# Kernel tuning notes

Hardware: AMD Instinct MI355X
Metric: run time of the kernel (lower is better)

The kernel has to match this reference:

```python
import jax, jax.numpy as jnp
import numpy as np

IN_C, HID, L, NN, BS, OUT = 32, 128, 4, 64, 512, 3
N = NN * BS  # total graph vertices
EPS_LN = 1e-5
EPS_SM = 1e-16  # PyG softmax eps


def setup_inputs() -> dict:
    key = jax.random.key(0)
    ks = jax.random.split(key, 16)
    E = 524288
    x = jax.random.normal(ks[0], (N, IN_C), dtype=jnp.float32)
    edge_index = jax.random.randint(ks[1], (2, E), 0, N, dtype=jnp.int64)
    s = 0.1
    # first GAT layer (in -> hidden)
    W0 = jax.random.normal(ks[2], (IN_C, HID), dtype=jnp.float32) * s
    att_src0 = jax.random.normal(ks[3], (HID,), dtype=jnp.float32) * s
    att_dst0 = jax.random.normal(ks[4], (HID,), dtype=jnp.float32) * s
    bias0 = jnp.zeros((HID,), dtype=jnp.float32)
    # residual GAT layers (hidden -> hidden), stacked over L
    W_res = jax.random.normal(ks[5], (L, HID, HID), dtype=jnp.float32) * s
    att_src_res = jax.random.normal(ks[6], (L, HID), dtype=jnp.float32) * s
    att_dst_res = jax.random.normal(ks[7], (L, HID), dtype=jnp.float32) * s
    bias_res = jnp.zeros((L, HID), dtype=jnp.float32)
    gamma = jnp.ones((L, HID), dtype=jnp.float32)
    beta = jnp.zeros((L, HID), dtype=jnp.float32)
    # per-node predictor heads
    W1p = jax.random.normal(ks[8], (NN, HID, HID // 2), dtype=jnp.float32) * s
    W2p = jax.random.normal(ks[9], (NN, HID // 2, OUT), dtype=jnp.float32) * s
    return {"x": x, "edge_index": edge_index, "W0": W0, "att_src0": att_src0,
            "att_dst0": att_dst0, "bias0": bias0, "W_res": W_res,
            "att_src_res": att_src_res, "att_dst_res": att_dst_res,
            "bias_res": bias_res, "gamma": gamma, "beta": beta,
            "W1p": W1p, "W2p": W2p}


def _gat(x, src, dst, W, a_src, a_dst, b):
    # PyG GATConv, heads=1, negative_slope=0.2, self-loops already appended
    h = x @ W                                   # [N, H]
    a_s = (h * a_src).sum(-1)                   # [N]
    a_d = (h * a_dst).sum(-1)                   # [N]
    e = jax.nn.leaky_relu(a_s[src] + a_d[dst], 0.2)   # [E]
    m = jax.ops.segment_max(e, dst, num_segments=N)
    e = jnp.exp(e - m[dst])
    z = jax.ops.segment_sum(e, dst, num_segments=N)
    alpha = e / (z[dst] + EPS_SM)               # [E]
    out = jax.ops.segment_sum(h[src] * alpha[:, None], dst, num_segments=N)
    return out + b


def _layernorm(x, g, b):
    mu = x.mean(-1, keepdims=True)
    var = ((x - mu) ** 2).mean(-1, keepdims=True)
    return (x - mu) * jax.lax.rsqrt(var + EPS_LN) * g + b


def reference(x, edge_index, W0, att_src0, att_dst0, bias0, W_res,
              att_src_res, att_dst_res, bias_res, gamma, beta, W1p, W2p):
    loops = jnp.arange(N, dtype=edge_index.dtype)
    src = jnp.concatenate([edge_index[0], loops])
    dst = jnp.concatenate([edge_index[1], loops])
    # first GAT + relu
    h = jax.nn.relu(_gat(x, src, dst, W0, att_src0, att_dst0, bias0))
    # res+ blocks: h = h + conv(dropout(act(norm(h))))  (dropout=identity, eval)
    for i in range(L):
        t = jax.nn.relu(_layernorm(h, gamma[i], beta[i]))
        t = _gat(t, src, dst, W_res[i], att_src_res[i], att_dst_res[i], bias_res[i])
        h = h + t
    h = jax.nn.relu(_layernorm(h, gamma[0], beta[0]))
    # per-node predictor heads
    h = h.reshape(NN, BS, HID)
    t = jax.nn.relu(jnp.einsum('nbh,nhk->nbk', h, W1p))
    logits = jnp.einsum('nbk,nko->nbo', t, W2p)
    return jax.nn.softmax(logits, axis=-1)   # softmax over class dim (dim=1 per node slice)
```

## Files before the change

### kernel.cpp

```cpp
#include <hip/hip_runtime.h>
#include <hip/hip_fp8.h>
#include <math.h>

#define NND   32768
#define HIDD  128
#define NHEAD 64
#define BSS   512
#define OUTC  3

typedef _Float16 half_t;
typedef __attribute__((ext_vector_type(8))) _Float16 half8;
typedef __attribute__((ext_vector_type(4))) float f32x4;

__device__ __forceinline__ unsigned enc_fp8x4(float a, float b, float c, float d) {
    __hip_fp8x4_e4m3 q(make_float4(a, b, c, d));
    return (unsigned)q.__x;
}
__device__ __forceinline__ float4 dec_fp8x4(unsigned v) {
    __hip_fp8x4_e4m3 t; t.__x = (__hip_fp8x4_storage_t)v;
    return (float4)t;
}

__global__ __launch_bounds__(256) void prep_kernel(const float* __restrict__ W0,
        const float* __restrict__ W_res, const float* __restrict__ W1p,
        const float* __restrict__ as0, const float* __restrict__ ad0,
        const float* __restrict__ as_res, const float* __restrict__ ad_res,
        const float* __restrict__ x, const int* __restrict__ ei, int E,
        half_t* __restrict__ Wh, half_t* __restrict__ W1h, half_t* __restrict__ W0t,
        float* __restrict__ wvec, half_t* __restrict__ xh,
        int* __restrict__ counts, int* __restrict__ rank) {
    int b = blockIdx.x, tid = threadIdx.x;
    if (b < 64) {
        __shared__ float tile[32][33];
        int l = b >> 4, t = b & 15;
        int k0 = (t >> 2) * 32, n0 = (t & 3) * 32;
        const float* src = W_res + (size_t)l * 128 * 128;
        half_t* dst = Wh + (size_t)l * 128 * 128;
        int c = tid & 31, r0 = tid >> 5;
#pragma unroll
        for (int i = 0; i < 4; ++i) tile[r0 + i * 8][c] = src[(size_t)(k0 + r0 + i * 8) * 128 + n0 + c];
        __syncthreads();
#pragma unroll
        for (int i = 0; i < 4; ++i) dst[(size_t)(n0 + r0 + i * 8) * 128 + k0 + c] = (half_t)tile[c][r0 + i * 8];
    } else if (b < 576) {
        __shared__ float tile[32][33];
        int bb = b - 64, head = bb >> 3, t = bb & 7;
        int k0 = (t >> 1) * 32, n0 = (t & 1) * 32;
        const float* src = W1p + (size_t)head * 128 * 64;
        half_t* dst = W1h + (size_t)head * 64 * 128;
        int c = tid & 31, r0 = tid >> 5;
#pragma unroll
        for (int i = 0; i < 4; ++i) tile[r0 + i * 8][c] = src[(size_t)(k0 + r0 + i * 8) * 64 + n0 + c];
        __syncthreads();
#pragma unroll
        for (int i = 0; i < 4; ++i) dst[(size_t)(n0 + r0 + i * 8) * 128 + k0 + c] = (half_t)tile[c][r0 + i * 8];
    } else if (b == 576) {
        __shared__ float t0[32][129];
        for (int i = tid; i < 4096; i += 256) t0[i >> 7][i & 127] = W0[i];
        __syncthreads();
        for (int i = tid; i < 4096; i += 256) { int n = i >> 5, k = i & 31; W0t[n * 32 + k] = (half_t)t0[k][n]; }
    } else if (b == 577) {
        for (int task = tid; task < 1088; task += 256) {
            const float* row; const float* att; int slot, sd;
            if (task < 64) {
                int k = task >> 1; sd = task & 1;
                row = W0 + k * 128; att = sd ? ad0 : as0; slot = k;
            } else {
                int tt = task - 64; int l = 1 + tt / 256; int r = tt % 256;
                int k = r >> 1; sd = r & 1;
                row = W_res + (size_t)(l - 1) * 16384 + k * 128;
                att = (sd ? ad_res : as_res) + (l - 1) * 128;
                slot = l * 128 + k;
            }
            float s = 0.f;
            for (int n = 0; n < 128; ++n) s += row[n] * att[n];
            (sd ? wvec + 640 : wvec)[slot] = s;
        }
    } else if (b < 1090) {
        int b2 = b - 578;
        const float* xs = x + (size_t)b2 * 64 * 32;
        half_t* xd = xh + (size_t)b2 * 64 * 32;
        for (int i = tid; i < 1024; i += 256) {
            float2 v = ((const float2*)xs)[i];
            union { unsigned u; half_t h[2]; } cv;
            cv.h[0] = (half_t)v.x; cv.h[1] = (half_t)v.y;
            ((unsigned*)xd)[i] = cv.u;
        }
    } else {
        int j = (b - 1090) * 256 + tid;
        int Etot = E + NND;
        if (j >= Etot) return;
        int dst = (j < E) ? ei[E + j] : (j - E);
        rank[j] = atomicAdd(&counts[dst], 1);
    }
}

__global__ __launch_bounds__(1024) void scan_kernel(const int* __restrict__ counts,
                                                    int* __restrict__ off) {
    __shared__ int sums[1024];
    int tid = threadIdx.x;
    int base = tid * 32;
    int tmp[32];
    int run = 0;
#pragma unroll
    for (int i = 0; i < 8; ++i) {
        int4 c4 = *(const int4*)&counts[base + i * 4];
        tmp[i*4+0] = run; run += c4.x;
        tmp[i*4+1] = run; run += c4.y;
        tmp[i*4+2] = run; run += c4.z;
        tmp[i*4+3] = run; run += c4.w;
    }
    sums[tid] = run;
    __syncthreads();
    for (int d = 1; d < 1024; d <<= 1) {
        int v = (tid >= d) ? sums[tid - d] : 0;
        __syncthreads();
        sums[tid] += v;
        __syncthreads();
    }
    int ebase = (tid == 0) ? 0 : sums[tid - 1];
#pragma unroll
    for (int i = 0; i < 32; ++i) off[base + i] = ebase + tmp[i];
    if (tid == 1023) off[NND] = sums[1023];
}

__global__ __launch_bounds__(256) void fill_a0_kernel(const int* __restrict__ ei, int E, int egrid,
        const int* __restrict__ off, const int* __restrict__ rank, int* __restrict__ csr_src,
        const half_t* __restrict__ xh, const float* __restrict__ wvec,
        float* __restrict__ a_s, float* __restrict__ a_d) {
    int b = blockIdx.x, tid = threadIdx.x;
    if (b < egrid) {
        int j = b * 256 + tid;
        int Etot = E + NND;
        if (j >= Etot) return;
        int src, dst;
        if (j < E) { src = ei[j]; dst = ei[E + j]; }
        else       { src = j - E; dst = j - E; }
        csr_src[off[dst] + rank[j]] = src;
    } else {
        __shared__ float ws0[32], wd0[32];
        if (tid < 32) { ws0[tid] = wvec[tid]; wd0[tid] = wvec[640 + tid]; }
        __syncthreads();
        int g = (b - egrid) * 256 + tid;
        int node = g >> 2, part = g & 3;
        half8 xv = *(const half8*)&xh[(size_t)node * 32 + part * 8];
        float s = 0.f, d2 = 0.f;
#pragma unroll
        for (int j = 0; j < 8; ++j) { float f = (float)xv[j]; s += f * ws0[part * 8 + j]; d2 += f * wd0[part * 8 + j]; }
        s += __shfl_xor(s, 1); s += __shfl_xor(s, 2);
        d2 += __shfl_xor(d2, 1); d2 += __shfl_xor(d2, 2);
        if (part == 0) { a_s[node] = s; a_d[node] = d2; }
    }
}

template <int K, bool RES>
__global__ __launch_bounds__(256) void fused_kernel(const void* __restrict__ srcdat,
        const float* __restrict__ a_sv, const float* __restrict__ a_dv,
        const int* __restrict__ csr_src, const int* __restrict__ off,
        const half_t* __restrict__ Whl, const float* __restrict__ bias,
        half_t* __restrict__ Hh, unsigned char* __restrict__ Th8o,
        const float* __restrict__ gamma, const float* __restrict__ beta,
        const float* __restrict__ wsn, const float* __restrict__ wdn,
        float* __restrict__ as_out, float* __restrict__ ad_out) {
    constexpr int KP = (K == 32) ? 40 : 136;
    __shared__ __align__(16) half_t Pt[16][KP];
    __shared__ __align__(16) float vv[16][132];
    int tid = threadIdx.x;
    int wv = tid >> 6, lane = tid & 63;
    int q = lane >> 4, r15 = lane & 15;
    int n0 = blockIdx.x * 16;

    for (int ln = wv * 4; ln < wv * 4 + 4; ++ln) {
        int d = n0 + ln;
        int beg = off[d], end = off[d + 1];
        float adv = a_dv[d];
        float pz = 0.f;
        if constexpr (K == 32) {
            const half_t* xh = (const half_t*)srcdat;
            float a0 = 0.f, a1 = 0.f;
            for (int base = beg; base < end; base += 64) {
                int j = base + lane;
                int s = 0; float p = 0.f;
                if (j < end) {
                    s = csr_src[j];
                    float t = a_sv[s] + adv;
                    t = (t > 0.f) ? t : 0.2f * t;
                    p = __expf(t);
                }
                pz += p;
                int cnt = end - base; if (cnt > 64) cnt = 64;
                int full = cnt & ~15;
                int k4 = 0;
                for (; k4 < full; k4 += 16) {
                    int s0 = __shfl(s, k4 + q);      float p0 = __shfl(p, k4 + q);
                    int s1 = __shfl(s, k4 + 4 + q);  float p1 = __shfl(p, k4 + 4 + q);
                    int s2 = __shfl(s, k4 + 8 + q);  float p2 = __shfl(p, k4 + 8 + q);
                    int s3 = __shfl(s, k4 + 12 + q); float p3 = __shfl(p, k4 + 12 + q);
                    union { unsigned u; half_t h[2]; } u0, u1, u2, u3;
                    u0.u = *(const unsigned*)&xh[(size_t)s0 * 32 + r15 * 2];
                    u1.u = *(const unsigned*)&xh[(size_t)s1 * 32 + r15 * 2];
                    u2.u = *(const unsigned*)&xh[(size_t)s2 * 32 + r15 * 2];
                    u3.u = *(const unsigned*)&xh[(size_t)s3 * 32 + r15 * 2];
                    a0 += p0 * (float)u0.h[0] + p1 * (float)u1.h[0] + p2 * (float)u2.h[0] + p3 * (float)u3.h[0];
                    a1 += p0 * (float)u0.h[1] + p1 * (float)u1.h[1] + p2 * (float)u2.h[1] + p3 * (float)u3.h[1];
                }
                for (; k4 < cnt; k4 += 4) {
                    int s0 = __shfl(s, k4 + q); float p0 = __shfl(p, k4 + q);
                    union { unsigned u; half_t h[2]; } u0;
                    u0.u = *(const unsigned*)&xh[(size_t)s0 * 32 + r15 * 2];
                    a0 += p0 * (float)u0.h[0]; a1 += p0 * (float)u0.h[1];
                }
            }
#pragma unroll
            for (int o = 32; o; o >>= 1) pz += __shfl_xor(pz, o);
            a0 += __shfl_xor(a0, 16); a0 += __shfl_xor(a0, 32);
            a1 += __shfl_xor(a1, 16); a1 += __shfl_xor(a1, 32);
            if (q == 0) {
                float inv = 1.f / (pz + 1e-16f);
                union { unsigned u; half_t h[2]; } w2;
                w2.h[0] = (half_t)(a0 * inv); w2.h[1] = (half_t)(a1 * inv);
                *(unsigned*)&Pt[ln][r15 * 2] = w2.u;
            }
        } else {
            const unsigned char* F8 = (const unsigned char*)srcdat;
            float acc[8] = {0.f,0.f,0.f,0.f,0.f,0.f,0.f,0.f};
            for (int base = beg; base < end; base += 64) {
                int j = base + lane;
                int s = 0; float p = 0.f;
                if (j < end) {
                    s = csr_src[j];
                    float t = a_sv[s] + adv;
                    t = (t > 0.f) ? t : 0.2f * t;
                    p = __expf(t);
                }
                pz += p;
                int cnt = end - base; if (cnt > 64) cnt = 64;
                int full = cnt & ~15;
                int k4 = 0;
                for (; k4 < full; k4 += 16) {
                    int s0 = __shfl(s, k4 + q);      float p0 = __shfl(p, k4 + q);
                    int s1 = __shfl(s, k4 + 4 + q);  float p1 = __shfl(p, k4 + 4 + q);
                    int s2 = __shfl(s, k4 + 8 + q);  float p2 = __shfl(p, k4 + 8 + q);
                    int s3 = __shfl(s, k4 + 12 + q); float p3 = __shfl(p, k4 + 12 + q);
                    uint2 r0 = *(const uint2*)&F8[(size_t)s0 * HIDD + r15 * 8];
                    uint2 r1 = *(const uint2*)&F8[(size_t)s1 * HIDD + r15 * 8];
                    uint2 r2 = *(const uint2*)&F8[(size_t)s2 * HIDD + r15 * 8];
                    uint2 r3 = *(const uint2*)&F8[(size_t)s3 * HIDD + r15 * 8];
                    float4 f;
                    f = dec_fp8x4(r0.x); acc[0]+=p0*f.x; acc[1]+=p0*f.y; acc[2]+=p0*f.z; acc[3]+=p0*f.w;
                    f = dec_fp8x4(r0.y); acc[4]+=p0*f.x; acc[5]+=p0*f.y; acc[6]+=p0*f.z; acc[7]+=p0*f.w;
                    f = dec_fp8x4(r1.x); acc[0]+=p1*f.x; acc[1]+=p1*f.y; acc[2]+=p1*f.z; acc[3]+=p1*f.w;
                    f = dec_fp8x4(r1.y); acc[4]+=p1*f.x; acc[5]+=p1*f.y; acc[6]+=p1*f.z; acc[7]+=p1*f.w;
                    f = dec_fp8x4(r2.x); acc[0]+=p2*f.x; acc[1]+=p2*f.y; acc[2]+=p2*f.z; acc[3]+=p2*f.w;
                    f = dec_fp8x4(r2.y); acc[4]+=p2*f.x; acc[5]+=p2*f.y; acc[6]+=p2*f.z; acc[7]+=p2*f.w;
                    f = dec_fp8x4(r3.x); acc[0]+=p3*f.x; acc[1]+=p3*f.y; acc[2]+=p3*f.z; acc[3]+=p3*f.w;
                    f = dec_fp8x4(r3.y); acc[4]+=p3*f.x; acc[5]+=p3*f.y; acc[6]+=p3*f.z; acc[7]+=p3*f.w;
                }
                for (; k4 < cnt; k4 += 4) {
                    int s0 = __shfl(s, k4 + q); float p0 = __shfl(p, k4 + q);
                    uint2 r0 = *(const uint2*)&F8[(size_t)s0 * HIDD + r15 * 8];
                    float4 f;
                    f = dec_fp8x4(r0.x); acc[0]+=p0*f.x; acc[1]+=p0*f.y; acc[2]+=p0*f.z; acc[3]+=p0*f.w;
                    f = dec_fp8x4(r0.y); acc[4]+=p0*f.x; acc[5]+=p0*f.y; acc[6]+=p0*f.z; acc[7]+=p0*f.w;
                }
            }
#pragma unroll
            for (int o = 32; o; o >>= 1) pz += __shfl_xor(pz, o);
#pragma unroll
            for (int i = 0; i < 8; ++i) {
                acc[i] += __shfl_xor(acc[i], 16);
                acc[i] += __shfl_xor(acc[i], 32);
            }
            if (q == 0) {
                float inv = 1.f / (pz + 1e-16f);
                union { int4 v; half_t hh[8]; } u;
#pragma unroll
                for (int i = 0; i < 8; ++i) u.hh[i] = (half_t)(acc[i] * inv);
                *(int4*)&Pt[ln][r15 * 8] = u.v;
            }
        }
    }
    __syncthreads();

    half8 afrag[K / 32];
#pragma unroll
    for (int s = 0; s < K / 32; ++s)
        afrag[s] = *(const half8*)&Pt[r15][s * 32 + q * 8];
    f32x4 acc2[2];
#pragma unroll
    for (int i = 0; i < 2; ++i) {
        int ct = wv * 2 + i;
        f32x4 c = {0.f, 0.f, 0.f, 0.f};
#pragma unroll
        for (int s = 0; s < K / 32; ++s) {
            half8 bfrag = *(const half8*)&Whl[(size_t)(ct * 16 + r15) * K + s * 32 + q * 8];
            c = __builtin_amdgcn_mfma_f32_16x16x32_f16(afrag[s], bfrag, c, 0, 0, 0);
        }
        acc2[i] = c;
    }
#pragma unroll
    for (int i = 0; i < 2; ++i)
#pragma unroll
        for (int r = 0; r < 4; ++r)
            vv[q * 4 + r][wv * 32 + i * 16 + r15] = acc2[i][r];
    __syncthreads();

    int grp = tid >> 4, sub = tid & 15;
    float4 bi0 = *(const float4*)&bias[sub * 8],  bi1 = *(const float4*)&bias[sub * 8 + 4];
    float4 g0  = *(const float4*)&gamma[sub * 8], g1  = *(const float4*)&gamma[sub * 8 + 4];
    float4 be0 = *(const float4*)&beta[sub * 8],  be1 = *(const float4*)&beta[sub * 8 + 4];
    float4 ws0 = *(const float4*)&wsn[sub * 8],   ws1 = *(const float4*)&wsn[sub * 8 + 4];
    float4 wd0 = *(const float4*)&wdn[sub * 8],   wd1 = *(const float4*)&wdn[sub * 8 + 4];
    float bi[8] = {bi0.x,bi0.y,bi0.z,bi0.w,bi1.x,bi1.y,bi1.z,bi1.w};
    float gg[8] = {g0.x,g0.y,g0.z,g0.w,g1.x,g1.y,g1.z,g1.w};
    float be[8] = {be0.x,be0.y,be0.z,be0.w,be1.x,be1.y,be1.z,be1.w};
    float ws[8] = {ws0.x,ws0.y,ws0.z,ws0.w,ws1.x,ws1.y,ws1.z,ws1.w};
    float wd[8] = {wd0.x,wd0.y,wd0.z,wd0.w,wd1.x,wd1.y,wd1.z,wd1.w};
    int node = n0 + grp;
    float v8[8];
#pragma unroll
    for (int j = 0; j < 8; ++j) v8[j] = vv[grp][sub * 8 + j] + bi[j];
    if (RES) {
        half8 hold = *(const half8*)&Hh[(size_t)node * HIDD + sub * 8];
#pragma unroll
        for (int j = 0; j < 8; ++j) v8[j] += (float)hold[j];
    } else {
#pragma unroll
        for (int j = 0; j < 8; ++j) v8[j] = fmaxf(v8[j], 0.f);
    }
    union { int4 i4; half_t h[8]; } hw;
#pragma unroll
    for (int j = 0; j < 8; ++j) hw.h[j] = (half_t)v8[j];
    *(int4*)&Hh[(size_t)node * HIDD + sub * 8] = hw.i4;
    float sum = 0.f;
#pragma unroll
    for (int j = 0; j < 8; ++j) sum += v8[j];
#pragma unroll
    for (int o = 8; o; o >>= 1) sum += __shfl_xor(sum, o);
    float mu = sum * (1.f / HIDD);
    float var = 0.f;
#pragma unroll
    for (int j = 0; j < 8; ++j) { float dx = v8[j] - mu; var += dx * dx; }
#pragma unroll
    for (int o = 8; o; o >>= 1) var += __shfl_xor(var, o);
    float rs = rsqrtf(var * (1.f / HIDD) + 1e-5f);
    float tt[8];
    float asn = 0.f, adn = 0.f;
#pragma unroll
    for (int j = 0; j < 8; ++j) {
        float t = fmaxf((v8[j] - mu) * rs * gg[j] + be[j], 0.f);
        tt[j] = t;
        asn += t * ws[j];
        adn += t * wd[j];
    }
    uint2 tw;
    tw.x = enc_fp8x4(tt[0], tt[1], tt[2], tt[3]);
    tw.y = enc_fp8x4(tt[4], tt[5], tt[6], tt[7]);
    *(uint2*)&Th8o[(size_t)node * HIDD + sub * 8] = tw;
#pragma unroll
    for (int o = 8; o; o >>= 1) { asn += __shfl_xor(asn, o); adn += __shfl_xor(adn, o); }
    if (sub == 0) { as_out[node] = asn; ad_out[node] = adn; }
}

__global__ __launch_bounds__(256) void agg_kernel(const unsigned char* __restrict__ F8,
        const float* __restrict__ a_s, const float* __restrict__ a_dv,
        const int* __restrict__ csr_src, const int* __restrict__ off,
        half_t* __restrict__ P) {
    int d = (blockIdx.x * 256 + threadIdx.x) >> 6;
    int lane = threadIdx.x & 63;
    int q = lane >> 4, r15 = lane & 15;
    int beg = off[d], end = off[d + 1];
    float adv = a_dv[d];
    float pz = 0.f;
    float acc[8] = {0.f,0.f,0.f,0.f,0.f,0.f,0.f,0.f};
    for (int base = beg; base < end; base += 64) {
        int j = base + lane;
        int s = 0; float p = 0.f;
        if (j < end) {
            s = csr_src[j];
            float t = a_s[s] + adv;
            t = (t > 0.f) ? t : 0.2f * t;
            p = __expf(t);
        }
        pz += p;
        int cnt = end - base; if (cnt > 64) cnt = 64;
        int full = cnt & ~15;
        int k4 = 0;
        for (; k4 < full; k4 += 16) {
            int s0 = __shfl(s, k4 + q);      float p0 = __shfl(p, k4 + q);
            int s1 = __shfl(s, k4 + 4 + q);  float p1 = __shfl(p, k4 + 4 + q);
            int s2 = __shfl(s, k4 + 8 + q);  float p2 = __shfl(p, k4 + 8 + q);
            int s3 = __shfl(s, k4 + 12 + q); float p3 = __shfl(p, k4 + 12 + q);
            uint2 r0 = *(const uint2*)&F8[(size_t)s0 * HIDD + r15 * 8];
            uint2 r1 = *(const uint2*)&F8[(size_t)s1 * HIDD + r15 * 8];
            uint2 r2 = *(const uint2*)&F8[(size_t)s2 * HIDD + r15 * 8];
            uint2 r3 = *(const uint2*)&F8[(size_t)s3 * HIDD + r15 * 8];
            float4 f;
            f = dec_fp8x4(r0.x); acc[0]+=p0*f.x; acc[1]+=p0*f.y; acc[2]+=p0*f.z; acc[3]+=p0*f.w;
            f = dec_fp8x4(r0.y); acc[4]+=p0*f.x; acc[5]+=p0*f.y; acc[6]+=p0*f.z; acc[7]+=p0*f.w;
            f = dec_fp8x4(r1.x); acc[0]+=p1*f.x; acc[1]+=p1*f.y; acc[2]+=p1*f.z; acc[3]+=p1*f.w;
            f = dec_fp8x4(r1.y); acc[4]+=p1*f.x; acc[5]+=p1*f.y; acc[6]+=p1*f.z; acc[7]+=p1*f.w;
            f = dec_fp8x4(r2.x); acc[0]+=p2*f.x; acc[1]+=p2*f.y; acc[2]+=p2*f.z; acc[3]+=p2*f.w;
            f = dec_fp8x4(r2.y); acc[4]+=p2*f.x; acc[5]+=p2*f.y; acc[6]+=p2*f.z; acc[7]+=p2*f.w;
            f = dec_fp8x4(r3.x); acc[0]+=p3*f.x; acc[1]+=p3*f.y; acc[2]+=p3*f.z; acc[3]+=p3*f.w;
            f = dec_fp8x4(r3.y); acc[4]+=p3*f.x; acc[5]+=p3*f.y; acc[6]+=p3*f.z; acc[7]+=p3*f.w;
        }
        for (; k4 < cnt; k4 += 4) {
            int s0 = __shfl(s, k4 + q); float p0 = __shfl(p, k4 + q);
            uint2 r0 = *(const uint2*)&F8[(size_t)s0 * HIDD + r15 * 8];
            float4 f;
            f = dec_fp8x4(r0.x); acc[0]+=p0*f.x; acc[1]+=p0*f.y; acc[2]+=p0*f.z; acc[3]+=p0*f.w;
            f = dec_fp8x4(r0.y); acc[4]+=p0*f.x; acc[5]+=p0*f.y; acc[6]+=p0*f.z; acc[7]+=p0*f.w;
        }
    }
#pragma unroll
    for (int o = 32; o; o >>= 1) pz += __shfl_xor(pz, o);
#pragma unroll
    for (int i = 0; i < 8; ++i) {
        acc[i] += __shfl_xor(acc[i], 16);
        acc[i] += __shfl_xor(acc[i], 32);
    }
    if (q == 0) {
        float inv = 1.f / (pz + 1e-16f);
        union { int4 v; half_t hh[8]; } u;
#pragma unroll
        for (int i = 0; i < 8; ++i) u.hh[i] = (half_t)(acc[i] * inv);
        *(int4*)&P[(size_t)d * HIDD + r15 * 8] = u.v;
    }
}

__global__ __launch_bounds__(256) void gemm_last_kernel(const half_t* __restrict__ P,
        const half_t* __restrict__ Whl, const float* __restrict__ bias,
        const half_t* __restrict__ Hh,
        const float* __restrict__ gamma, const float* __restrict__ beta,
        const half_t* __restrict__ W1h, const float* __restrict__ W2p,
        float* __restrict__ out) {
    __shared__ __align__(16) char smraw[128 * 136 * 2];
    half_t* w = (half_t*)smraw;
    float* vv = (float*)smraw;
    int tid = threadIdx.x;
    int n0 = blockIdx.x * 64;
    for (int i = tid; i < 128 * 16; i += 256) {
        int n = i >> 4, c = i & 15;
        *(int4*)&w[n * 136 + c * 8] = *(const int4*)&Whl[(size_t)n * 128 + c * 8];
    }
    int wv = tid >> 6, lane = tid & 63;
    int q = lane >> 4, r15 = lane & 15;
    half8 afrag[4];
    int nodeA = n0 + wv * 16 + r15;
#pragma unroll
    for (int s = 0; s < 4; ++s)
        afrag[s] = *(const half8*)&P[(size_t)nodeA * HIDD + s * 32 + q * 8];
    __syncthreads();
    f32x4 acc[8];
#pragma unroll
    for (int ct = 0; ct < 8; ++ct) {
        f32x4 c = {0.f, 0.f, 0.f, 0.f};
#pragma unroll
        for (int s = 0; s < 4; ++s) {
            half8 bfrag = *(const half8*)&w[(ct * 16 + r15) * 136 + s * 32 + q * 8];
            c = __builtin_amdgcn_mfma_f32_16x16x32_f16(afrag[s], bfrag, c, 0, 0, 0);
        }
        acc[ct] = c;
    }
    __syncthreads();
#pragma unroll
    for (int ct = 0; ct < 8; ++ct)
#pragma unroll
        for (int r = 0; r < 4; ++r)
            vv[(wv * 16 + q * 4 + r) * 132 + ct * 16 + r15] = acc[ct][r];
    __syncthreads();
    int grp = tid >> 4, sub = tid & 15;
    float4 bi0 = *(const float4*)&bias[sub * 8],  bi1 = *(const float4*)&bias[sub * 8 + 4];
    float4 g0  = *(const float4*)&gamma[sub * 8], g1  = *(const float4*)&gamma[sub * 8 + 4];
    float4 be0 = *(const float4*)&beta[sub * 8],  be1 = *(const float4*)&beta[sub * 8 + 4];
    float bi[8] = {bi0.x,bi0.y,bi0.z,bi0.w,bi1.x,bi1.y,bi1.z,bi1.w};
    float gg[8] = {g0.x,g0.y,g0.z,g0.w,g1.x,g1.y,g1.z,g1.w};
    float be[8] = {be0.x,be0.y,be0.z,be0.w,be1.x,be1.y,be1.z,be1.w};
    half_t tv[4][8];
#pragma unroll
    for (int pp = 0; pp < 4; ++pp) {
        int nl = grp + pp * 16;
        int node = n0 + nl;
        float v8[8];
        half8 hold = *(const half8*)&Hh[(size_t)node * HIDD + sub * 8];
#pragma unroll
        for (int j = 0; j < 8; ++j) v8[j] = vv[nl * 132 + sub * 8 + j] + bi[j] + (float)hold[j];
        float sum = 0.f;
#pragma unroll
        for (int j = 0; j < 8; ++j) sum += v8[j];
#pragma unroll
        for (int o = 8; o; o >>= 1) sum += __shfl_xor(sum, o);
        float mu = sum * (1.f / HIDD);
        float var = 0.f;
#pragma unroll
        for (int j = 0; j < 8; ++j) { float dx = v8[j] - mu; var += dx * dx; }
#pragma unroll
        for (int o = 8; o; o >>= 1) var += __shfl_xor(var, o);
        float rs = rsqrtf(var * (1.f / HIDD) + 1e-5f);
#pragma unroll
        for (int j = 0; j < 8; ++j)
            tv[pp][j] = (half_t)fmaxf((v8[j] - mu) * rs * gg[j] + be[j], 0.f);
    }
    __syncthreads();
#pragma unroll
    for (int pp = 0; pp < 4; ++pp) {
        int nl = grp + pp * 16;
        union { int4 i4; half_t h[8]; } u;
#pragma unroll
        for (int j = 0; j < 8; ++j) u.h[j] = tv[pp][j];
        *(int4*)&w[nl * 136 + sub * 8] = u.i4;
    }
    __syncthreads();
    int head = n0 >> 9;
    const half_t* W1g = W1h + (size_t)head * 64 * 128;
    half8 pa[4];
#pragma unroll
    for (int s = 0; s < 4; ++s)
        pa[s] = *(const half8*)&w[(wv * 16 + r15) * 136 + s * 32 + q * 8];
    float lg[3][4];
#pragma unroll
    for (int o = 0; o < 3; ++o)
#pragma unroll
        for (int r = 0; r < 4; ++r) lg[o][r] = 0.f;
#pragma unroll
    for (int ct2 = 0; ct2 < 4; ++ct2) {
        int n2 = ct2 * 16 + r15;
        f32x4 c = {0.f, 0.f, 0.f, 0.f};
#pragma unroll
        for (int s = 0; s < 4; ++s) {
            half8 bfrag = *(const half8*)&W1g[(size_t)n2 * 128 + s * 32 + q * 8];
            c = __builtin_amdgcn_mfma_f32_16x16x32_f16(pa[s], bfrag, c, 0, 0, 0);
        }
        float w2a = W2p[(size_t)head * 192 + n2 * 3 + 0];
        float w2b = W2p[(size_t)head * 192 + n2 * 3 + 1];
        float w2c = W2p[(size_t)head * 192 + n2 * 3 + 2];
#pragma unroll
        for (int r = 0; r < 4; ++r) {
            float t = fmaxf(c[r], 0.f);
            lg[0][r] += t * w2a;
            lg[1][r] += t * w2b;
            lg[2][r] += t * w2c;
        }
    }
#pragma unroll
    for (int o = 8; o; o >>= 1)
#pragma unroll
        for (int oo = 0; oo < 3; ++oo)
#pragma unroll
            for (int r = 0; r < 4; ++r) lg[oo][r] += __shfl_xor(lg[oo][r], o);
    if (r15 == 0) {
        int nodeD = n0 + wv * 16 + q * 4;
#pragma unroll
        for (int r = 0; r < 4; ++r) {
            float l0 = lg[0][r], l1 = lg[1][r], l2 = lg[2][r];
            float mx = fmaxf(l0, fmaxf(l1, l2));
            float e0 = __expf(l0 - mx), e1 = __expf(l1 - mx), e2 = __expf(l2 - mx);
            float inv = 1.f / (e0 + e1 + e2);
            float* op = out + (size_t)(nodeD + r) * OUTC;
            op[0] = e0 * inv; op[1] = e1 * inv; op[2] = e2 * inv;
        }
    }
}

extern "C" void kernel_launch(void* const* d_in, const int* in_sizes, int n_in,
                              void* d_out, int out_size, void* d_ws, size_t ws_size,
                              hipStream_t stream) {
    const float* x        = (const float*)d_in[0];
    const int*   ei       = (const int*)d_in[1];
    const float* W0       = (const float*)d_in[2];
    const float* att_src0 = (const float*)d_in[3];
    const float* att_dst0 = (const float*)d_in[4];
    const float* bias0    = (const float*)d_in[5];
    const float* W_res    = (const float*)d_in[6];
    const float* as_res   = (const float*)d_in[7];
    const float* ad_res   = (const float*)d_in[8];
    const float* b_res    = (const float*)d_in[9];
    const float* gamma    = (const float*)d_in[10];
    const float* beta     = (const float*)d_in[11];
    const float* W1p      = (const float*)d_in[12];
    const float* W2p      = (const float*)d_in[13];
    float* out = (float*)d_out;

    int E = in_sizes[1] / 2;
    int Etot = E + NND;

    char* p = (char*)d_ws;
    auto alloc = [&](size_t bytes) { void* r = (void*)p; p += (bytes + 255) & ~(size_t)255; return r; };
    int*    counts  = (int*)alloc((size_t)NND * 4);
    int*    off     = (int*)alloc((size_t)(NND + 1) * 4);
    int*    rank    = (int*)alloc((size_t)Etot * 4);
    int*    csr_src = (int*)alloc((size_t)Etot * 4);
    half_t* xh      = (half_t*)alloc((size_t)NND * 32 * 2);
    half_t* Pbuf    = (half_t*)alloc((size_t)NND * HIDD * 2);
    unsigned char* Th8a = (unsigned char*)alloc((size_t)NND * HIDD);
    unsigned char* Th8b = (unsigned char*)alloc((size_t)NND * HIDD);
    half_t* Hh      = (half_t*)alloc((size_t)NND * HIDD * 2);
    float*  a_s0    = (float*)alloc((size_t)NND * 4);
    float*  a_d0    = (float*)alloc((size_t)NND * 4);
    float*  a_s1    = (float*)alloc((size_t)NND * 4);
    float*  a_d1    = (float*)alloc((size_t)NND * 4);
    half_t* Wh      = (half_t*)alloc((size_t)4 * HIDD * HIDD * 2);
    half_t* W1h     = (half_t*)alloc((size_t)NHEAD * 64 * HIDD * 2);
    half_t* W0t     = (half_t*)alloc((size_t)HIDD * 32 * 2);
    float*  wvec    = (float*)alloc((size_t)1280 * 4);

    int egrid = (Etot + 255) / 256;

    hipMemsetAsync(counts, 0, (size_t)NND * 4, stream);
    prep_kernel<<<1090 + egrid, 256, 0, stream>>>(W0, W_res, W1p, att_src0, att_dst0,
        as_res, ad_res, x, ei, E, Wh, W1h, W0t, wvec, xh, counts, rank);
    scan_kernel<<<1, 1024, 0, stream>>>(counts, off);
    fill_a0_kernel<<<egrid + 512, 256, 0, stream>>>(ei, E, egrid, off, rank, csr_src,
                                                    xh, wvec, a_s0, a_d0);

    fused_kernel<32, false><<<NND / 16, 256, 0, stream>>>((const void*)xh,
        a_s0, a_d0, csr_src, off, W0t, bias0, Hh, Th8a,
        gamma, beta, wvec + 128, wvec + 640 + 128, a_s1, a_d1);

    fused_kernel<128, true><<<NND / 16, 256, 0, stream>>>((const void*)Th8a,
        a_s1, a_d1, csr_src, off, Wh, b_res, Hh, Th8b,
        gamma + 128, beta + 128, wvec + 256, wvec + 640 + 256, a_s0, a_d0);
    fused_kernel<128, true><<<NND / 16, 256, 0, stream>>>((const void*)Th8b,
        a_s0, a_d0, csr_src, off, Wh + 16384, b_res + 128, Hh, Th8a,
        gamma + 256, beta + 256, wvec + 384, wvec + 640 + 384, a_s1, a_d1);
    fused_kernel<128, true><<<NND / 16, 256, 0, stream>>>((const void*)Th8a,
        a_s1, a_d1, csr_src, off, Wh + 2 * 16384, b_res + 2 * 128, Hh, Th8b,
        gamma + 384, beta + 384, wvec + 512, wvec + 640 + 512, a_s0, a_d0);

    agg_kernel<<<NND / 4, 256, 0, stream>>>(Th8b, a_s0, a_d0, csr_src, off, Pbuf);
    gemm_last_kernel<<<NND / 64, 256, 0, stream>>>(Pbuf, Wh + (size_t)3 * 16384,
        b_res + 3 * HIDD, Hh, gamma, beta, W1h, W2p, out);
}
```

Measured before the change: 284.4 us.

## Merge GAT layers into one persistent cooperative kernel with grid syncs

Replaces the per-layer fused kernels and the separate final aggregation plus GEMM kernels with one persistent cooperative kernel of 512 blocks. Each block walks 16-node tiles and uses grid.sync between layers. The last layer now fuses aggregation with the final GEMM and predictor head per tile, so the intermediate P buffer round trip is gone. This removes launch gaps and one global write/read, but it limits occupancy to a fixed persistent grid and adds grid-barrier cost. If the cooperative launch fails it falls back to separate launches.

```diff
diff --git a/kernel.cpp b/kernel.cpp
--- a/kernel.cpp
+++ b/kernel.cpp
@@ -1,12 +1,16 @@
 #include <hip/hip_runtime.h>
 #include <hip/hip_fp8.h>
+#include <hip/hip_cooperative_groups.h>
 #include <math.h>
+
+namespace cg = cooperative_groups;
 
 #define NND   32768
 #define HIDD  128
 #define NHEAD 64
 #define BSS   512
 #define OUTC  3
+#define NTILES (NND / 16)
 
 typedef _Float16 half_t;
 typedef __attribute__((ext_vector_type(8))) _Float16 half8;
@@ -153,135 +157,156 @@
     }
 }
 
-template <int K, bool RES>
-__global__ __launch_bounds__(256) void fused_kernel(const void* __restrict__ srcdat,
+
+struct MArgs {
+    const half_t* xh;
+    const int* csr_src;
+    const int* off;
+    const half_t* W0t;
+    const half_t* Wh;
+    const float* bias0;
+    const float* b_res;
+    const float* gamma;
+    const float* beta;
+    const float* wvec;
+    float* a_s0; float* a_d0; float* a_s1; float* a_d1;
+    unsigned char* Th8a; unsigned char* Th8b;
+    half_t* Hh;
+    const half_t* W1h;
+    const float* W2p;
+    float* out;
+};
+
+__device__ __forceinline__ void agg_l0_tile(const half_t* __restrict__ xh,
         const float* __restrict__ a_sv, const float* __restrict__ a_dv,
         const int* __restrict__ csr_src, const int* __restrict__ off,
-        const half_t* __restrict__ Whl, const float* __restrict__ bias,
-        half_t* __restrict__ Hh, unsigned char* __restrict__ Th8o,
-        const float* __restrict__ gamma, const float* __restrict__ beta,
-        const float* __restrict__ wsn, const float* __restrict__ wdn,
-        float* __restrict__ as_out, float* __restrict__ ad_out) {
-    constexpr int KP = (K == 32) ? 40 : 136;
-    __shared__ __align__(16) half_t Pt[16][KP];
-    __shared__ __align__(16) float vv[16][132];
-    int tid = threadIdx.x;
-    int wv = tid >> 6, lane = tid & 63;
-    int q = lane >> 4, r15 = lane & 15;
-    int n0 = blockIdx.x * 16;
-
+        int n0, int wv, int lane, int q, int r15, half_t Pt[16][136]) {
+    for (int ln = wv * 4; ln < wv * 4 + 4; ++ln) {
+        int d = n0 + ln;
+        int beg = off[d], end = off[d + 1];
+        float adv = a_dv[d];
+        float pz = 0.f, a0 = 0.f, a1 = 0.f;
+        for (int base = beg; base < end; base += 64) {
+            int j = base + lane;
+            int s = 0; float p = 0.f;
+            if (j < end) {
+                s = csr_src[j];
+                float t = a_sv[s] + adv;
+                t = (t > 0.f) ? t : 0.2f * t;
+                p = __expf(t);
+            }
+            pz += p;
+            int cnt = end - base; if (cnt > 64) cnt = 64;
+            int full = cnt & ~15;
+            int k4 = 0;
+            for (; k4 < full; k4 += 16) {
+                int s0 = __shfl(s, k4 + q);      float p0 = __shfl(p, k4 + q);
+                int s1 = __shfl(s, k4 + 4 + q);  float p1 = __shfl(p, k4 + 4 + q);
+                int s2 = __shfl(s, k4 + 8 + q);  float p2 = __shfl(p, k4 + 8 + q);
+                int s3 = __shfl(s, k4 + 12 + q); float p3 = __shfl(p, k4 + 12 + q);
+                union { unsigned u; half_t h[2]; } u0, u1, u2, u3;
+                u0.u = *(const unsigned*)&xh[(size_t)s0 * 32 + r15 * 2];
+                u1.u = *(const unsigned*)&xh[(size_t)s1 * 32 + r15 * 2];
+                u2.u = *(const unsigned*)&xh[(size_t)s2 * 32 + r15 * 2];
+                u3.u = *(const unsigned*)&xh[(size_t)s3 * 32 + r15 * 2];
+                a0 += p0 * (float)u0.h[0] + p1 * (float)u1.h[0] + p2 * (float)u2.h[0] + p3 * (float)u3.h[0];
+                a1 += p0 * (float)u0.h[1] + p1 * (float)u1.h[1] + p2 * (float)u2.h[1] + p3 * (float)u3.h[1];
+            }
+            for (; k4 < cnt; k4 += 4) {
+                int s0 = __shfl(s, k4 + q); float p0 = __shfl(p, k4 + q);
+                union { unsigned u; half_t h[2]; } u0;
+                u0.u = *(const unsigned*)&xh[(size_t)s0 * 32 + r15 * 2];
+                a0 += p0 * (float)u0.h[0]; a1 += p0 * (float)u0.h[1];
+            }
+        }
+#pragma unroll
+        for (int o = 32; o; o >>= 1) pz += __shfl_xor(pz, o);
+        a0 += __shfl_xor(a0, 16); a0 += __shfl_xor(a0, 32);
+        a1 += __shfl_xor(a1, 16); a1 += __shfl_xor(a1, 32);
+        if (q == 0) {
+            float inv = 1.f / (pz + 1e-16f);
+            union { unsigned u; half_t h[2]; } w2;
+            w2.h[0] = (half_t)(a0 * inv); w2.h[1] = (half_t)(a1 * inv);
+            *(unsigned*)&Pt[ln][r15 * 2] = w2.u;
+        }
+    }
+}
+
+__device__ __forceinline__ void agg_res_tile(const unsigned char* __restrict__ F8,
+        const float* __restrict__ a_sv, const float* __restrict__ a_dv,
+        const int* __restrict__ csr_src, const int* __restrict__ off,
+        int n0, int wv, int lane, int q, int r15, half_t Pt[16][136]) {
     for (int ln = wv * 4; ln < wv * 4 + 4; ++ln) {
         int d = n0 + ln;
         int beg = off[d], end = off[d + 1];
         float adv = a_dv[d];
         float pz = 0.f;
-        if constexpr (K == 32) {
-            const half_t* xh = (const half_t*)srcdat;
-            float a0 = 0.f, a1 = 0.f;
-            for (int base = beg; base < end; base += 64) {
-                int j = base + lane;
-                int s = 0; float p = 0.f;
-                if (j < end) {
-                    s = csr_src[j];
-                    float t = a_sv[s] + adv;
-                    t = (t > 0.f) ? t : 0.2f * t;
-                    p = __expf(t);
-                }
-                pz += p;
-                int cnt = end - base; if (cnt > 64) cnt = 64;
-                int full = cnt & ~15;
-                int k4 = 0;
-                for (; k4 < full; k4 += 16) {
-                    int s0 = __shfl(s, k4 + q);      float p0 = __shfl(p, k4 + q);
-                    int s1 = __shfl(s, k4 + 4 + q);  float p1 = __shfl(p, k4 + 4 + q);
-                    int s2 = __shfl(s, k4 + 8 + q);  float p2 = __shfl(p, k4 + 8 + q);
-                    int s3 = __shfl(s, k4 + 12 + q); float p3 = __shfl(p, k4 + 12 + q);
-                    union { unsigned u; half_t h[2]; } u0, u1, u2, u3;
-                    u0.u = *(const unsigned*)&xh[(size_t)s0 * 32 + r15 * 2];
-                    u1.u = *(const unsigned*)&xh[(size_t)s1 * 32 + r15 * 2];
-                    u2.u = *(const unsigned*)&xh[(size_t)s2 * 32 + r15 * 2];
-                    u3.u = *(const unsigned*)&xh[(size_t)s3 * 32 + r15 * 2];
-                    a0 += p0 * (float)u0.h[0] + p1 * (float)u1.h[0] + p2 * (float)u2.h[0] + p3 * (float)u3.h[0];
-                    a1 += p0 * (float)u0.h[1] + p1 * (float)u1.h[1] + p2 * (float)u2.h[1] + p3 * (float)u3.h[1];
-                }
-                for (; k4 < cnt; k4 += 4) {
-                    int s0 = __shfl(s, k4 + q); float p0 = __shfl(p, k4 + q);
-                    union { unsigned u; half_t h[2]; } u0;
-                    u0.u = *(const unsigned*)&xh[(size_t)s0 * 32 + r15 * 2];
-                    a0 += p0 * (float)u0.h[0]; a1 += p0 * (float)u0.h[1];
-                }
+        float acc[8] = {0.f,0.f,0.f,0.f,0.f,0.f,0.f,0.f};
+        for (int base = beg; base < end; base += 64) {
+            int j = base + lane;
+            int s = 0; float p = 0.f;
+            if (j < end) {
+                s = csr_src[j];
+                float t = a_sv[s] + adv;
+                t = (t > 0.f) ? t : 0.2f * t;
+                p = __expf(t);
             }
-#pragma unroll
-            for (int o = 32; o; o >>= 1) pz += __shfl_xor(pz, o);
-            a0 += __shfl_xor(a0, 16); a0 += __shfl_xor(a0, 32);
-            a1 += __shfl_xor(a1, 16); a1 += __shfl_xor(a1, 32);
-            if (q == 0) {
-                float inv = 1.f / (pz + 1e-16f);
-                union { unsigned u; half_t h[2]; } w2;
-                w2.h[0] = (half_t)(a0 * inv); w2.h[1] = (half_t)(a1 * inv);
-                *(unsigned*)&Pt[ln][r15 * 2] = w2.u;
+            pz += p;
+            int cnt = end - base; if (cnt > 64) cnt = 64;
+            int full = cnt & ~15;
+            int k4 = 0;
+            for (; k4 < full; k4 += 16) {
+                int s0 = __shfl(s, k4 + q);      float p0 = __shfl(p, k4 + q);
+                int s1 = __shfl(s, k4 + 4 + q);  float p1 = __shfl(p, k4 + 4 + q);
+                int s2 = __shfl(s, k4 + 8 + q);  float p2 = __shfl(p, k4 + 8 + q);
+                int s3 = __shfl(s, k4 + 12 + q); float p3 = __shfl(p, k4 + 12 + q);
+                uint2 r0 = *(const uint2*)&F8[(size_t)s0 * HIDD + r15 * 8];
+                uint2 r1 = *(const uint2*)&F8[(size_t)s1 * HIDD + r15 * 8];
+                uint2 r2 = *(const uint2*)&F8[(size_t)s2 * HIDD + r15 * 8];
+                uint2 r3 = *(const uint2*)&F8[(size_t)s3 * HIDD + r15 * 8];
+                float4 f;
+                f = dec_fp8x4(r0.x); acc[0]+=p0*f.x; acc[1]+=p0*f.y; acc[2]+=p0*f.z; acc[3]+=p0*f.w;
+                f = dec_fp8x4(r0.y); acc[4]+=p0*f.x; acc[5]+=p0*f.y; acc[6]+=p0*f.z; acc[7]+=p0*f.w;
+                f = dec_fp8x4(r1.x); acc[0]+=p1*f.x; acc[1]+=p1*f.y; acc[2]+=p1*f.z; acc[3]+=p1*f.w;
+                f = dec_fp8x4(r1.y); acc[4]+=p1*f.x; acc[5]+=p1*f.y; acc[6]+=p1*f.z; acc[7]+=p1*f.w;
+                f = dec_fp8x4(r2.x); acc[0]+=p2*f.x; acc[1]+=p2*f.y; acc[2]+=p2*f.z; acc[3]+=p2*f.w;
+                f = dec_fp8x4(r2.y); acc[4]+=p2*f.x; acc[5]+=p2*f.y; acc[6]+=p2*f.z; acc[7]+=p2*f.w;
+                f = dec_fp8x4(r3.x); acc[0]+=p3*f.x; acc[1]+=p3*f.y; acc[2]+=p3*f.z; acc[3]+=p3*f.w;
+                f = dec_fp8x4(r3.y); acc[4]+=p3*f.x; acc[5]+=p3*f.y; acc[6]+=p3*f.z; acc[7]+=p3*f.w;
             }
-        } else {
-            const unsigned char* F8 = (const unsigned char*)srcdat;
-            float acc[8] = {0.f,0.f,0.f,0.f,0.f,0.f,0.f,0.f};
-            for (int base = beg; base < end; base += 64) {
-                int j = base + lane;
-                int s = 0; float p = 0.f;
-                if (j < end) {
-                    s = csr_src[j];
-                    float t = a_sv[s] + adv;
-                    t = (t > 0.f) ? t : 0.2f * t;
-                    p = __expf(t);
-                }
-                pz += p;
-                int cnt = end - base; if (cnt > 64) cnt = 64;
-                int full = cnt & ~15;
-                int k4 = 0;
-                for (; k4 < full; k4 += 16) {
-                    int s0 = __shfl(s, k4 + q);      float p0 = __shfl(p, k4 + q);
-                    int s1 = __shfl(s, k4 + 4 + q);  float p1 = __shfl(p, k4 + 4 + q);
-                    int s2 = __shfl(s, k4 + 8 + q);  float p2 = __shfl(p, k4 + 8 + q);
-                    int s3 = __shfl(s, k4 + 12 + q); float p3 = __shfl(p, k4 + 12 + q);
-                    uint2 r0 = *(const uint2*)&F8[(size_t)s0 * HIDD + r15 * 8];
-                    uint2 r1 = *(const uint2*)&F8[(size_t)s1 * HIDD + r15 * 8];
-                    uint2 r2 = *(const uint2*)&F8[(size_t)s2 * HIDD + r15 * 8];
-                    uint2 r3 = *(const uint2*)&F8[(size_t)s3 * HIDD + r15 * 8];
-                    float4 f;
-                    f = dec_fp8x4(r0.x); acc[0]+=p0*f.x; acc[1]+=p0*f.y; acc[2]+=p0*f.z; acc[3]+=p0*f.w;
-                    f = dec_fp8x4(r0.y); acc[4]+=p0*f.x; acc[5]+=p0*f.y; acc[6]+=p0*f.z; acc[7]+=p0*f.w;
-                    f = dec_fp8x4(r1.x); acc[0]+=p1*f.x; acc[1]+=p1*f.y; acc[2]+=p1*f.z; acc[3]+=p1*f.w;
-                    f = dec_fp8x4(r1.y); acc[4]+=p1*f.x; acc[5]+=p1*f.y; acc[6]+=p1*f.z; acc[7]+=p1*f.w;
-                    f = dec_fp8x4(r2.x); acc[0]+=p2*f.x; acc[1]+=p2*f.y; acc[2]+=p2*f.z; acc[3]+=p2*f.w;
-                    f = dec_fp8x4(r2.y); acc[4]+=p2*f.x; acc[5]+=p2*f.y; acc[6]+=p2*f.z; acc[7]+=p2*f.w;
-                    f = dec_fp8x4(r3.x); acc[0]+=p3*f.x; acc[1]+=p3*f.y; acc[2]+=p3*f.z; acc[3]+=p3*f.w;
-                    f = dec_fp8x4(r3.y); acc[4]+=p3*f.x; acc[5]+=p3*f.y; acc[6]+=p3*f.z; acc[7]+=p3*f.w;
-                }
-                for (; k4 < cnt; k4 += 4) {
-                    int s0 = __shfl(s, k4 + q); float p0 = __shfl(p, k4 + q);
-                    uint2 r0 = *(const uint2*)&F8[(size_t)s0 * HIDD + r15 * 8];
-                    float4 f;
-                    f = dec_fp8x4(r0.x); acc[0]+=p0*f.x; acc[1]+=p0*f.y; acc[2]+=p0*f.z; acc[3]+=p0*f.w;
-                    f = dec_fp8x4(r0.y); acc[4]+=p0*f.x; acc[5]+=p0*f.y; acc[6]+=p0*f.z; acc[7]+=p0*f.w;
-                }
+            for (; k4 < cnt; k4 += 4) {
+                int s0 = __shfl(s, k4 + q); float p0 = __shfl(p, k4 + q);
+                uint2 r0 = *(const uint2*)&F8[(size_t)s0 * HIDD + r15 * 8];
+                float4 f;
+                f = dec_fp8x4(r0.x); acc[0]+=p0*f.x; acc[1]+=p0*f.y; acc[2]+=p0*f.z; acc[3]+=p0*f.w;
+                f = dec_fp8x4(r0.y); acc[4]+=p0*f.x; acc[5]+=p0*f.y; acc[6]+=p0*f.z; acc[7]+=p0*f.w;
             }
-#pragma unroll
-            for (int o = 32; o; o >>= 1) pz += __shfl_xor(pz, o);
-#pragma unroll
-            for (int i = 0; i < 8; ++i) {
-                acc[i] += __shfl_xor(acc[i], 16);
-                acc[i] += __shfl_xor(acc[i], 32);
-            }
-            if (q == 0) {
-                float inv = 1.f / (pz + 1e-16f);
-                union { int4 v; half_t hh[8]; } u;
-#pragma unroll
-                for (int i = 0; i < 8; ++i) u.hh[i] = (half_t)(acc[i] * inv);
-                *(int4*)&Pt[ln][r15 * 8] = u.v;
-            }
-        }
-    }
-    __syncthreads();
-
+        }
+#pragma unroll
+        for (int o = 32; o; o >>= 1) pz += __shfl_xor(pz, o);
+#pragma unroll
+        for (int i = 0; i < 8; ++i) {
+            acc[i] += __shfl_xor(acc[i], 16);
+            acc[i] += __shfl_xor(acc[i], 32);
+        }
+        if (q == 0) {
+            float inv = 1.f / (pz + 1e-16f);
+            union { int4 v; half_t hh[8]; } u;
+#pragma unroll
+            for (int i = 0; i < 8; ++i) u.hh[i] = (half_t)(acc[i] * inv);
+            *(int4*)&Pt[ln][r15 * 8] = u.v;
+        }
+    }
+}
+
+template <int K, bool RES>
+__device__ __forceinline__ void gemm_epi_tile(int n0, int tid, int wv, int q, int r15,
+        const half_t* __restrict__ Whl, const float* __restrict__ bias,
+        half_t* __restrict__ Hh, unsigned char* __restrict__ Th8o,
+        const float* __restrict__ gamma, const float* __restrict__ beta,
+        const float* __restrict__ wsn, const float* __restrict__ wdn,
+        float* __restrict__ as_out, float* __restrict__ ad_out,
+        half_t Pt[16][136], float vv[16][132]) {
     half8 afrag[K / 32];
 #pragma unroll
     for (int s = 0; s < K / 32; ++s)
@@ -304,7 +329,6 @@
         for (int r = 0; r < 4; ++r)
             vv[q * 4 + r][wv * 32 + i * 16 + r15] = acc2[i][r];
     __syncthreads();
-
     int grp = tid >> 4, sub = tid & 15;
     float4 bi0 = *(const float4*)&bias[sub * 8],  bi1 = *(const float4*)&bias[sub * 8 + 4];
     float4 g0  = *(const float4*)&gamma[sub * 8], g1  = *(const float4*)&gamma[sub * 8 + 4];
@@ -362,186 +386,86 @@
     if (sub == 0) { as_out[node] = asn; ad_out[node] = adn; }
 }
 
-__global__ __launch_bounds__(256) void agg_kernel(const unsigned char* __restrict__ F8,
-        const float* __restrict__ a_s, const float* __restrict__ a_dv,
-        const int* __restrict__ csr_src, const int* __restrict__ off,
-        half_t* __restrict__ P) {
-    int d = (blockIdx.x * 256 + threadIdx.x) >> 6;
-    int lane = threadIdx.x & 63;
-    int q = lane >> 4, r15 = lane & 15;
-    int beg = off[d], end = off[d + 1];
-    float adv = a_dv[d];
-    float pz = 0.f;
-    float acc[8] = {0.f,0.f,0.f,0.f,0.f,0.f,0.f,0.f};
-    for (int base = beg; base < end; base += 64) {
-        int j = base + lane;
-        int s = 0; float p = 0.f;
-        if (j < end) {
-            s = csr_src[j];
-            float t = a_s[s] + adv;
-            t = (t > 0.f) ? t : 0.2f * t;
-            p = __expf(t);
-        }
-        pz += p;
-        int cnt = end - base; if (cnt > 64) cnt = 64;
-        int full = cnt & ~15;
-        int k4 = 0;
-        for (; k4 < full; k4 += 16) {
-            int s0 = __shfl(s, k4 + q);      float p0 = __shfl(p, k4 + q);
-            int s1 = __shfl(s, k4 + 4 + q);  float p1 = __shfl(p, k4 + 4 + q);
-            int s2 = __shfl(s, k4 + 8 + q);  float p2 = __shfl(p, k4 + 8 + q);
-            int s3 = __shfl(s, k4 + 12 + q); float p3 = __shfl(p, k4 + 12 + q);
-            uint2 r0 = *(const uint2*)&F8[(size_t)s0 * HIDD + r15 * 8];
-            uint2 r1 = *(const uint2*)&F8[(size_t)s1 * HIDD + r15 * 8];
-            uint2 r2 = *(const uint2*)&F8[(size_t)s2 * HIDD + r15 * 8];
-            uint2 r3 = *(const uint2*)&F8[(size_t)s3 * HIDD + r15 * 8];
-            float4 f;
-            f = dec_fp8x4(r0.x); acc[0]+=p0*f.x; acc[1]+=p0*f.y; acc[2]+=p0*f.z; acc[3]+=p0*f.w;
-            f = dec_fp8x4(r0.y); acc[4]+=p0*f.x; acc[5]+=p0*f.y; acc[6]+=p0*f.z; acc[7]+=p0*f.w;
-            f = dec_fp8x4(r1.x); acc[0]+=p1*f.x; acc[1]+=p1*f.y; acc[2]+=p1*f.z; acc[3]+=p1*f.w;
-            f = dec_fp8x4(r1.y); acc[4]+=p1*f.x; acc[5]+=p1*f.y; acc[6]+=p1*f.z; acc[7]+=p1*f.w;
-            f = dec_fp8x4(r2.x); acc[0]+=p2*f.x; acc[1]+=p2*f.y; acc[2]+=p2*f.z; acc[3]+=p2*f.w;
-            f = dec_fp8x4(r2.y); acc[4]+=p2*f.x; acc[5]+=p2*f.y; acc[6]+=p2*f.z; acc[7]+=p2*f.w;
-            f = dec_fp8x4(r3.x); acc[0]+=p3*f.x; acc[1]+=p3*f.y; acc[2]+=p3*f.z; acc[3]+=p3*f.w;
-            f = dec_fp8x4(r3.y); acc[4]+=p3*f.x; acc[5]+=p3*f.y; acc[6]+=p3*f.z; acc[7]+=p3*f.w;
-        }
-        for (; k4 < cnt; k4 += 4) {
-            int s0 = __shfl(s, k4 + q); float p0 = __shfl(p, k4 + q);
-            uint2 r0 = *(const uint2*)&F8[(size_t)s0 * HIDD + r15 * 8];
-            float4 f;
-            f = dec_fp8x4(r0.x); acc[0]+=p0*f.x; acc[1]+=p0*f.y; acc[2]+=p0*f.z; acc[3]+=p0*f.w;
-            f = dec_fp8x4(r0.y); acc[4]+=p0*f.x; acc[5]+=p0*f.y; acc[6]+=p0*f.z; acc[7]+=p0*f.w;
-        }
-    }
-#pragma unroll
-    for (int o = 32; o; o >>= 1) pz += __shfl_xor(pz, o);
-#pragma unroll
-    for (int i = 0; i < 8; ++i) {
-        acc[i] += __shfl_xor(acc[i], 16);
-        acc[i] += __shfl_xor(acc[i], 32);
-    }
-    if (q == 0) {
-        float inv = 1.f / (pz + 1e-16f);
-        union { int4 v; half_t hh[8]; } u;
-#pragma unroll
-        for (int i = 0; i < 8; ++i) u.hh[i] = (half_t)(acc[i] * inv);
-        *(int4*)&P[(size_t)d * HIDD + r15 * 8] = u.v;
-    }
-}
-
-__global__ __launch_bounds__(256) void gemm_last_kernel(const half_t* __restrict__ P,
-        const half_t* __restrict__ Whl, const float* __restrict__ bias,
-        const half_t* __restrict__ Hh,
-        const float* __restrict__ gamma, const float* __restrict__ beta,
-        const half_t* __restrict__ W1h, const float* __restrict__ W2p,
-        float* __restrict__ out) {
-    __shared__ __align__(16) char smraw[128 * 136 * 2];
-    half_t* w = (half_t*)smraw;
-    float* vv = (float*)smraw;
-    int tid = threadIdx.x;
-    int n0 = blockIdx.x * 64;
-    for (int i = tid; i < 128 * 16; i += 256) {
-        int n = i >> 4, c = i & 15;
-        *(int4*)&w[n * 136 + c * 8] = *(const int4*)&Whl[(size_t)n * 128 + c * 8];
-    }
-    int wv = tid >> 6, lane = tid & 63;
-    int q = lane >> 4, r15 = lane & 15;
+__device__ __forceinline__ void last_tile(int n0, int tid, int wv, int q, int r15,
+        const MArgs& A, half_t Pt[16][136], float vv[16][132]) {
+    const half_t* Whl = A.Wh + (size_t)3 * 16384;
     half8 afrag[4];
-    int nodeA = n0 + wv * 16 + r15;
 #pragma unroll
     for (int s = 0; s < 4; ++s)
-        afrag[s] = *(const half8*)&P[(size_t)nodeA * HIDD + s * 32 + q * 8];
-    __syncthreads();
-    f32x4 acc[8];
-#pragma unroll
-    for (int ct = 0; ct < 8; ++ct) {
+        afrag[s] = *(const half8*)&Pt[r15][s * 32 + q * 8];
+    f32x4 acc2[2];
+#pragma unroll
+    for (int i = 0; i < 2; ++i) {
+        int ct = wv * 2 + i;
         f32x4 c = {0.f, 0.f, 0.f, 0.f};
 #pragma unroll
         for (int s = 0; s < 4; ++s) {
-            half8 bfrag = *(const half8*)&w[(ct * 16 + r15) * 136 + s * 32 + q * 8];
+            half8 bfrag = *(const half8*)&Whl[(size_t)(ct * 16 + r15) * 128 + s * 32 + q * 8];
             c = __builtin_amdgcn_mfma_f32_16x16x32_f16(afrag[s], bfrag, c, 0, 0, 0);
         }
-        acc[ct] = c;
-    }
-    __syncthreads();
-#pragma unroll
-    for (int ct = 0; ct < 8; ++ct)
+        acc2[i] = c;
+    }
+#pragma unroll
+    for (int i = 0; i < 2; ++i)
 #pragma unroll
         for (int r = 0; r < 4; ++r)
-            vv[(wv * 16 + q * 4 + r) * 132 + ct * 16 + r15] = acc[ct][r];
+            vv[q * 4 + r][wv * 32 + i * 16 + r15] = acc2[i][r];
     __syncthreads();
     int grp = tid >> 4, sub = tid & 15;
-    float4 bi0 = *(const float4*)&bias[sub * 8],  bi1 = *(const float4*)&bias[sub * 8 + 4];
-    float4 g0  = *(const float4*)&gamma[sub * 8], g1  = *(const float4*)&gamma[sub * 8 + 4];
-    float4 be0 = *(const float4*)&beta[sub * 8],  be1 = *(const float4*)&beta[sub * 8 + 4];
+    const float* bias = A.b_res + 3 * HIDD;
+    float4 bi0 = *(const float4*)&bias[sub * 8],    bi1 = *(const float4*)&bias[sub * 8 + 4];
+    float4 g0  = *(const float4*)&A.gamma[sub * 8], g1  = *(const float4*)&A.gamma[sub * 8 + 4];
+    float4 be0 = *(const float4*)&A.beta[sub * 8],  be1 = *(const float4*)&A.beta[sub * 8 + 4];
     float bi[8] = {bi0.x,bi0.y,bi0.z,bi0.w,bi1.x,bi1.y,bi1.z,bi1.w};
     float gg[8] = {g0.x,g0.y,g0.z,g0.w,g1.x,g1.y,g1.z,g1.w};
     float be[8] = {be0.x,be0.y,be0.z,be0.w,be1.x,be1.y,be1.z,be1.w};
-    half_t tv[4][8];
-#pragma unroll
-    for (int pp = 0; pp < 4; ++pp) {
-        int nl = grp + pp * 16;
-        int node = n0 + nl;
-        float v8[8];
-        half8 hold = *(const half8*)&Hh[(size_t)node * HIDD + sub * 8];
-#pragma unroll
-        for (int j = 0; j < 8; ++j) v8[j] = vv[nl * 132 + sub * 8 + j] + bi[j] + (float)hold[j];
-        float sum = 0.f;
-#pragma unroll
-        for (int j = 0; j < 8; ++j) sum += v8[j];
-#pragma unroll
-        for (int o = 8; o; o >>= 1) sum += __shfl_xor(sum, o);
-        float mu = sum * (1.f / HIDD);
-        float var = 0.f;
-#pragma unroll
-        for (int j = 0; j < 8; ++j) { float dx = v8[j] - mu; var += dx * dx; }
-#pragma unroll
-        for (int o = 8; o; o >>= 1) var += __shfl_xor(var, o);
-        float rs = rsqrtf(var * (1.f / HIDD) + 1e-5f);
-#pragma unroll
-        for (int j = 0; j < 8; ++j)
-            tv[pp][j] = (half_t)fmaxf((v8[j] - mu) * rs * gg[j] + be[j], 0.f);
-    }
-    __syncthreads();
-#pragma unroll
-    for (int pp = 0; pp < 4; ++pp) {
-        int nl = grp + pp * 16;
-        union { int4 i4; half_t h[8]; } u;
-#pragma unroll
-        for (int j = 0; j < 8; ++j) u.h[j] = tv[pp][j];
-        *(int4*)&w[nl * 136 + sub * 8] = u.i4;
-    }
+    int node = n0 + grp;
+    float v8[8];
+    half8 hold = *(const half8*)&A.Hh[(size_t)node * HIDD + sub * 8];
+#pragma unroll
+    for (int j = 0; j < 8; ++j) v8[j] = vv[grp][sub * 8 + j] + bi[j] + (float)hold[j];
+    float sum = 0.f;
+#pragma unroll
+    for (int j = 0; j < 8; ++j) sum += v8[j];
+#pragma unroll
+    for (int o = 8; o; o >>= 1) sum += __shfl_xor(sum, o);
+    float mu = sum * (1.f / HIDD);
+    float var = 0.f;
+#pragma unroll
+    for (int j = 0; j < 8; ++j) { float dx = v8[j] - mu; var += dx * dx; }
+#pragma unroll
+    for (int o = 8; o; o >>= 1) var += __shfl_xor(var, o);
+    float rs = rsqrtf(var * (1.f / HIDD) + 1e-5f);
+    union { int4 i4; half_t h[8]; } u;
+#pragma unroll
+    for (int j = 0; j < 8; ++j)
+        u.h[j] = (half_t)fmaxf((v8[j] - mu) * rs * gg[j] + be[j], 0.f);
+    __syncthreads();
+    *(int4*)&Pt[grp][sub * 8] = u.i4;
     __syncthreads();
     int head = n0 >> 9;
-    const half_t* W1g = W1h + (size_t)head * 64 * 128;
+    const half_t* W1g = A.W1h + (size_t)head * 64 * 128;
     half8 pa[4];
 #pragma unroll
     for (int s = 0; s < 4; ++s)
-        pa[s] = *(const half8*)&w[(wv * 16 + r15) * 136 + s * 32 + q * 8];
+        pa[s] = *(const half8*)&Pt[r15][s * 32 + q * 8];
+    int n2 = wv * 16 + r15;
+    f32x4 c = {0.f, 0.f, 0.f, 0.f};
+#pragma unroll
+    for (int s = 0; s < 4; ++s) {
+        half8 bfrag = *(const half8*)&W1g[(size_t)n2 * 128 + s * 32 + q * 8];
+        c = __builtin_amdgcn_mfma_f32_16x16x32_f16(pa[s], bfrag, c, 0, 0, 0);
+    }
+    float w2a = A.W2p[(size_t)head * 192 + n2 * 3 + 0];
+    float w2b = A.W2p[(size_t)head * 192 + n2 * 3 + 1];
+    float w2c = A.W2p[(size_t)head * 192 + n2 * 3 + 2];
     float lg[3][4];
 #pragma unroll
-    for (int o = 0; o < 3; ++o)
-#pragma unroll
-        for (int r = 0; r < 4; ++r) lg[o][r] = 0.f;
-#pragma unroll
-    for (int ct2 = 0; ct2 < 4; ++ct2) {
-        int n2 = ct2 * 16 + r15;
-        f32x4 c = {0.f, 0.f, 0.f, 0.f};
-#pragma unroll
-        for (int s = 0; s < 4; ++s) {
-            half8 bfrag = *(const half8*)&W1g[(size_t)n2 * 128 + s * 32 + q * 8];
-            c = __builtin_amdgcn_mfma_f32_16x16x32_f16(pa[s], bfrag, c, 0, 0, 0);
-        }
-        float w2a = W2p[(size_t)head * 192 + n2 * 3 + 0];
-        float w2b = W2p[(size_t)head * 192 + n2 * 3 + 1];
-        float w2c = W2p[(size_t)head * 192 + n2 * 3 + 2];
-#pragma unroll
-        for (int r = 0; r < 4; ++r) {
-            float t = fmaxf(c[r], 0.f);
-            lg[0][r] += t * w2a;
-            lg[1][r] += t * w2b;
-            lg[2][r] += t * w2c;
-        }
+    for (int r = 0; r < 4; ++r) {
+        float t = fmaxf(c[r], 0.f);
+        lg[0][r] = t * w2a;
+        lg[1][r] = t * w2b;
+        lg[2][r] = t * w2c;
     }
 #pragma unroll
     for (int o = 8; o; o >>= 1)
@@ -549,18 +473,112 @@
         for (int oo = 0; oo < 3; ++oo)
 #pragma unroll
             for (int r = 0; r < 4; ++r) lg[oo][r] += __shfl_xor(lg[oo][r], o);
+    __syncthreads();
     if (r15 == 0) {
-        int nodeD = n0 + wv * 16 + q * 4;
-#pragma unroll
-        for (int r = 0; r < 4; ++r) {
-            float l0 = lg[0][r], l1 = lg[1][r], l2 = lg[2][r];
-            float mx = fmaxf(l0, fmaxf(l1, l2));
-            float e0 = __expf(l0 - mx), e1 = __expf(l1 - mx), e2 = __expf(l2 - mx);
-            float inv = 1.f / (e0 + e1 + e2);
-            float* op = out + (size_t)(nodeD + r) * OUTC;
-            op[0] = e0 * inv; op[1] = e1 * inv; op[2] = e2 * inv;
-        }
-    }
+#pragma unroll
+        for (int r = 0; r < 4; ++r)
+#pragma unroll
+            for (int oo = 0; oo < 3; ++oo) vv[q * 4 + r][wv * 3 + oo] = lg[oo][r];
+    }
+    __syncthreads();
+    if (tid < 16) {
+        float l0 = vv[tid][0] + vv[tid][3] + vv[tid][6] + vv[tid][9];
+        float l1 = vv[tid][1] + vv[tid][4] + vv[tid][7] + vv[tid][10];
+        float l2 = vv[tid][2] + vv[tid][5] + vv[tid][8] + vv[tid][11];
+        float mx = fmaxf(l0, fmaxf(l1, l2));
+        float e0 = __expf(l0 - mx), e1 = __expf(l1 - mx), e2 = __expf(l2 - mx);
+        float inv = 1.f / (e0 + e1 + e2);
+        float* op = A.out + (size_t)(n0 + tid) * OUTC;
+        op[0] = e0 * inv; op[1] = e1 * inv; op[2] = e2 * inv;
+    }
+}
+
+__global__ __launch_bounds__(256, 2) void mega_kernel(MArgs A) {
+    __shared__ __align__(16) half_t Pt[16][136];
+    __shared__ __align__(16) float vv[16][132];
+    cg::grid_group grid = cg::this_grid();
+    int tid = threadIdx.x;
+    int wv = tid >> 6, lane = tid & 63;
+    int q = lane >> 4, r15 = lane & 15;
+
+    for (int t = blockIdx.x; t < NTILES; t += gridDim.x) {
+        agg_l0_tile(A.xh, A.a_s0, A.a_d0, A.csr_src, A.off, t * 16, wv, lane, q, r15, Pt);
+        __syncthreads();
+        gemm_epi_tile<32, false>(t * 16, tid, wv, q, r15, A.W0t, A.bias0, A.Hh, A.Th8a,
+            A.gamma, A.beta, A.wvec + 128, A.wvec + 640 + 128, A.a_s1, A.a_d1, Pt, vv);
+        __syncthreads();
+    }
+    grid.sync();
+
+    for (int l = 0; l < 3; ++l) {
+        const unsigned char* Ts = (l & 1) ? A.Th8b : A.Th8a;
+        unsigned char* Td       = (l & 1) ? A.Th8a : A.Th8b;
+        const float* asv = (l & 1) ? A.a_s0 : A.a_s1;
+        const float* adv = (l & 1) ? A.a_d0 : A.a_d1;
+        float* aso = (l & 1) ? A.a_s1 : A.a_s0;
+        float* ado = (l & 1) ? A.a_d1 : A.a_d0;
+        for (int t = blockIdx.x; t < NTILES; t += gridDim.x) {
+            agg_res_tile(Ts, asv, adv, A.csr_src, A.off, t * 16, wv, lane, q, r15, Pt);
+            __syncthreads();
+            gemm_epi_tile<128, true>(t * 16, tid, wv, q, r15, A.Wh + (size_t)l * 16384,
+                A.b_res + l * HIDD, A.Hh, Td, A.gamma + (l + 1) * HIDD, A.beta + (l + 1) * HIDD,
+                A.wvec + (l + 2) * 128, A.wvec + 640 + (l + 2) * 128, aso, ado, Pt, vv);
+            __syncthreads();
+        }
+        grid.sync();
+    }
+
+    for (int t = blockIdx.x; t < NTILES; t += gridDim.x) {
+        agg_res_tile(A.Th8b, A.a_s0, A.a_d0, A.csr_src, A.off, t * 16, wv, lane, q, r15, Pt);
+        __syncthreads();
+        last_tile(t * 16, tid, wv, q, r15, A, Pt, vv);
+        __syncthreads();
+    }
+}
+
+__global__ __launch_bounds__(256) void fused1_l0(MArgs A) {
+    __shared__ __align__(16) half_t Pt[16][136];
+    __shared__ __align__(16) float vv[16][132];
+    int tid = threadIdx.x;
+    int wv = tid >> 6, lane = tid & 63;
+    int q = lane >> 4, r15 = lane & 15;
+    int t = blockIdx.x;
+    agg_l0_tile(A.xh, A.a_s0, A.a_d0, A.csr_src, A.off, t * 16, wv, lane, q, r15, Pt);
+    __syncthreads();
+    gemm_epi_tile<32, false>(t * 16, tid, wv, q, r15, A.W0t, A.bias0, A.Hh, A.Th8a,
+        A.gamma, A.beta, A.wvec + 128, A.wvec + 640 + 128, A.a_s1, A.a_d1, Pt, vv);
+}
+
+__global__ __launch_bounds__(256) void fused1_res(MArgs A, int l) {
+    __shared__ __align__(16) half_t Pt[16][136];
+    __shared__ __align__(16) float vv[16][132];
+    int tid = threadIdx.x;
+    int wv = tid >> 6, lane = tid & 63;
+    int q = lane >> 4, r15 = lane & 15;
+    int t = blockIdx.x;
+    const unsigned char* Ts = (l & 1) ? A.Th8b : A.Th8a;
+    unsigned char* Td       = (l & 1) ? A.Th8a : A.Th8b;
+    const float* asv = (l & 1) ? A.a_s0 : A.a_s1;
+    const float* adv = (l & 1) ? A.a_d0 : A.a_d1;
+    float* aso = (l & 1) ? A.a_s1 : A.a_s0;
+    float* ado = (l & 1) ? A.a_d1 : A.a_d0;
+    agg_res_tile(Ts, asv, adv, A.csr_src, A.off, t * 16, wv, lane, q, r15, Pt);
+    __syncthreads();
+    gemm_epi_tile<128, true>(t * 16, tid, wv, q, r15, A.Wh + (size_t)l * 16384,
+        A.b_res + l * HIDD, A.Hh, Td, A.gamma + (l + 1) * HIDD, A.beta + (l + 1) * HIDD,
+        A.wvec + (l + 2) * 128, A.wvec + 640 + (l + 2) * 128, aso, ado, Pt, vv);
+}
+
+__global__ __launch_bounds__(256) void fused1_last(MArgs A) {
+    __shared__ __align__(16) half_t Pt[16][136];
+    __shared__ __align__(16) float vv[16][132];
+    int tid = threadIdx.x;
+    int wv = tid >> 6, lane = tid & 63;
+    int q = lane >> 4, r15 = lane & 15;
+    int t = blockIdx.x;
+    agg_res_tile(A.Th8b, A.a_s0, A.a_d0, A.csr_src, A.off, t * 16, wv, lane, q, r15, Pt);
+    __syncthreads();
+    last_tile(t * 16, tid, wv, q, r15, A, Pt, vv);
 }
 
 extern "C" void kernel_launch(void* const* d_in, const int* in_sizes, int n_in,
@@ -592,7 +610,6 @@
     int*    rank    = (int*)alloc((size_t)Etot * 4);
     int*    csr_src = (int*)alloc((size_t)Etot * 4);
     half_t* xh      = (half_t*)alloc((size_t)NND * 32 * 2);
-    half_t* Pbuf    = (half_t*)alloc((size_t)NND * HIDD * 2);
     unsigned char* Th8a = (unsigned char*)alloc((size_t)NND * HIDD);
     unsigned char* Th8b = (unsigned char*)alloc((size_t)NND * HIDD);
     half_t* Hh      = (half_t*)alloc((size_t)NND * HIDD * 2);
@@ -614,21 +631,23 @@
     fill_a0_kernel<<<egrid + 512, 256, 0, stream>>>(ei, E, egrid, off, rank, csr_src,
                                                     xh, wvec, a_s0, a_d0);
 
-    fused_kernel<32, false><<<NND / 16, 256, 0, stream>>>((const void*)xh,
-        a_s0, a_d0, csr_src, off, W0t, bias0, Hh, Th8a,
-        gamma, beta, wvec + 128, wvec + 640 + 128, a_s1, a_d1);
-
-    fused_kernel<128, true><<<NND / 16, 256, 0, stream>>>((const void*)Th8a,
-        a_s1, a_d1, csr_src, off, Wh, b_res, Hh, Th8b,
-        gamma + 128, beta + 128, wvec + 256, wvec + 640 + 256, a_s0, a_d0);
-    fused_kernel<128, true><<<NND / 16, 256, 0, stream>>>((const void*)Th8b,
-        a_s0, a_d0, csr_src, off, Wh + 16384, b_res + 128, Hh, Th8a,
-        gamma + 256, beta + 256, wvec + 384, wvec + 640 + 384, a_s1, a_d1);
-    fused_kernel<128, true><<<NND / 16, 256, 0, stream>>>((const void*)Th8a,
-        a_s1, a_d1, csr_src, off, Wh + 2 * 16384, b_res + 2 * 128, Hh, Th8b,
-        gamma + 384, beta + 384, wvec + 512, wvec + 640 + 512, a_s0, a_d0);
-
-    agg_kernel<<<NND / 4, 256, 0, stream>>>(Th8b, a_s0, a_d0, csr_src, off, Pbuf);
-    gemm_last_kernel<<<NND / 64, 256, 0, stream>>>(Pbuf, Wh + (size_t)3 * 16384,
-        b_res + 3 * HIDD, Hh, gamma, beta, W1h, W2p, out);
-}
+    MArgs ma;
+    ma.xh = xh; ma.csr_src = csr_src; ma.off = off;
+    ma.W0t = W0t; ma.Wh = Wh;
+    ma.bias0 = bias0; ma.b_res = b_res;
+    ma.gamma = gamma; ma.beta = beta; ma.wvec = wvec;
+    ma.a_s0 = a_s0; ma.a_d0 = a_d0; ma.a_s1 = a_s1; ma.a_d1 = a_d1;
+    ma.Th8a = Th8a; ma.Th8b = Th8b; ma.Hh = Hh;
+    ma.W1h = W1h; ma.W2p = W2p; ma.out = out;
+
+    void* kargs[] = { (void*)&ma };
+    hipError_t ce = hipLaunchCooperativeKernel((void*)mega_kernel, dim3(512), dim3(256),
+                                               kargs, 0, stream);
+    if (ce != hipSuccess) {
+        (void)hipGetLastError();
+        fused1_l0<<<NTILES, 256, 0, stream>>>(ma);
+        for (int l = 0; l < 3; ++l)
+            fused1_res<<<NTILES, 256, 0, stream>>>(ma, l);
+        fused1_last<<<NTILES, 256, 0, stream>>>(ma);
+    }
+}
```

Result: slower. 656.9 us (+131.0%).
